# Optimization experiments

Measured on AMD Instinct MI355X. Metric: run time of the kernel, lower is better.

Reference implementation:

```python
import jax, jax.numpy as jnp
import numpy as np

N = 50000      # nodes
E = 800000     # edges (before self-loops)
F_IN = 256     # num_features
H = 4          # heads
C = 64         # hidden_channels
HC = H * C     # 256
L = 2          # n_layers
G = 128        # num graphs
DENSE = 64     # dense_nhid
NCLS = 2       # num_classes
NEG_SLOPE = 0.2
BN_EPS = 1e-5


def setup_inputs() -> dict:
    key = jax.random.key(0)
    ks = jax.random.split(key, 16)
    s = 0.1
    inp = {}
    inp['x'] = jax.random.normal(ks[0], (N, F_IN), jnp.float32)
    inp['edge_index'] = jax.random.randint(ks[1], (2, E), 0, N, dtype=jnp.int32)
    inp['batch'] = jnp.sort(jax.random.randint(ks[2], (N,), 0, G, dtype=jnp.int32))
    # conv1 (GATConv: lin weight [in, H*C], att vectors [H, C], bias [H*C])
    inp['W1'] = jax.random.normal(ks[3], (F_IN, HC), jnp.float32) * s
    inp['as1'] = jax.random.normal(ks[4], (H, C), jnp.float32) * s
    inp['ad1'] = jax.random.normal(ks[5], (H, C), jnp.float32) * s
    inp['b1'] = jnp.zeros((HC,), jnp.float32)
    # stacked params for the L inner conv layers + their BatchNorms
    inp['Wl'] = jax.random.normal(ks[6], (L, HC, HC), jnp.float32) * s
    inp['asl'] = jax.random.normal(ks[7], (L, H, C), jnp.float32) * s
    inp['adl'] = jax.random.normal(ks[8], (L, H, C), jnp.float32) * s
    inp['bl'] = jnp.zeros((L, HC), jnp.float32)
    inp['bng'] = jnp.ones((L, HC), jnp.float32)
    inp['bnb'] = jnp.zeros((L, HC), jnp.float32)
    # bn1 + MLP head
    inp['bn1g'] = jnp.ones((HC,), jnp.float32)
    inp['bn1b'] = jnp.zeros((HC,), jnp.float32)
    inp['lin1W'] = jax.random.normal(ks[9], (HC, DENSE), jnp.float32) * s
    inp['lin1b'] = jnp.zeros((DENSE,), jnp.float32)
    inp['lin2W'] = jax.random.normal(ks[10], (DENSE, DENSE), jnp.float32) * s
    inp['lin2b'] = jnp.zeros((DENSE,), jnp.float32)
    inp['lin3W'] = jax.random.normal(ks[11], (DENSE, NCLS), jnp.float32) * s
    inp['lin3b'] = jnp.zeros((NCLS,), jnp.float32)
    return inp


def _gat(x, src, dst, W, a_src, a_dst, b):
    # GATConv: h_j = W x_j; e_ij = LeakyReLU(a_src.h_j + a_dst.h_i);
    # alpha = softmax over incoming edges of node i; out_i = sum_j alpha*h_j (concat heads) + bias
    h = (x @ W).reshape(-1, H, C)                       # [N, H, C]
    es = jnp.sum(h * a_src, axis=-1)                    # [N, H]
    ed = jnp.sum(h * a_dst, axis=-1)                    # [N, H]
    e = jax.nn.leaky_relu(es[src] + ed[dst], NEG_SLOPE) # [E2, H]
    m = jax.ops.segment_max(e, dst, num_segments=N)
    ex = jnp.exp(e - m[dst])
    ssum = jax.ops.segment_sum(ex, dst, num_segments=N)
    alpha = ex / (ssum[dst] + 1e-16)                    # [E2, H]
    agg = jax.ops.segment_sum(h[src] * alpha[:, :, None], dst, num_segments=N)
    return agg.reshape(-1, HC) + b


def _bn(x, g, b):
    # BatchNorm1d in training mode (biased batch variance)
    mu = jnp.mean(x, axis=0)
    var = jnp.mean((x - mu) ** 2, axis=0)
    return (x - mu) / jnp.sqrt(var + BN_EPS) * g + b


def reference(x, edge_index, batch, W1, as1, ad1, b1, Wl, asl, adl, bl, bng, bnb,
              bn1g, bn1b, lin1W, lin1b, lin2W, lin2b, lin3W, lin3b):
    loops = jnp.arange(N, dtype=edge_index.dtype)
    src = jnp.concatenate([edge_index[0], loops])  # GATConv adds self-loops
    dst = jnp.concatenate([edge_index[1], loops])
    h = jax.nn.relu(_gat(x, src, dst, W1, as1, ad1, b1))
    for i in range(L):
        h = jax.nn.relu(_bn(_gat(h, src, dst, Wl[i], asl[i], adl[i], bl[i]), bng[i], bnb[i]))
    cnt = jax.ops.segment_sum(jnp.ones((N,), h.dtype), batch, num_segments=G)
    pooled = jax.ops.segment_sum(h, batch, num_segments=G) / jnp.maximum(cnt, 1.0)[:, None]
    z = _bn(pooled, bn1g, bn1b)  # dropout is identity in eval
    z = jax.nn.relu(z @ lin1W + lin1b)
    z = jax.nn.relu(z @ lin2W + lin2b)
    z = jax.nn.relu(z @ lin3W + lin3b)
    out = jax.nn.softmax(z, axis=1)
    return (out, pooled)
```

## Files before the change

kernel.cpp:

```cpp
#include <hip/hip_runtime.h>

#define N_NODES 50000
#define E_EDGES 800000
#define E2 (E_EDGES + N_NODES)
#define HC 256
#define NHEAD 4
#define GG 128
#define DENSE 64
#define NCLS 2
#define BN_EPS 1e-5f
#define NEG_SLOPE 0.2f
#define NEG_BIG -1e30f

typedef __attribute__((ext_vector_type(8))) short bf16x8;
typedef __attribute__((ext_vector_type(4))) float f32x4;

__device__ __forceinline__ unsigned short f2bf(float f) {
    unsigned int u = __float_as_uint(f);
    u = (u + 0x7FFFu + ((u >> 16) & 1u)) >> 16;
    return (unsigned short)u;
}
__device__ __forceinline__ float bf2f(unsigned short h) {
    return __uint_as_float(((unsigned int)h) << 16);
}
__device__ __forceinline__ float lrelu(float e) {
    return (e >= 0.f) ? e : NEG_SLOPE * e;
}
__device__ __forceinline__ void accum8(float acc[8], uint4 v, float w) {
    acc[0] = fmaf(w, __uint_as_float(v.x << 16), acc[0]);
    acc[1] = fmaf(w, __uint_as_float(v.x & 0xffff0000u), acc[1]);
    acc[2] = fmaf(w, __uint_as_float(v.y << 16), acc[2]);
    acc[3] = fmaf(w, __uint_as_float(v.y & 0xffff0000u), acc[3]);
    acc[4] = fmaf(w, __uint_as_float(v.z << 16), acc[4]);
    acc[5] = fmaf(w, __uint_as_float(v.z & 0xffff0000u), acc[5]);
    acc[6] = fmaf(w, __uint_as_float(v.w << 16), acc[6]);
    acc[7] = fmaf(w, __uint_as_float(v.w & 0xffff0000u), acc[7]);
}

__global__ __launch_bounds__(256) void convert_bf16_kernel(const float* __restrict__ in,
                                                           unsigned short* __restrict__ out,
                                                           int n8) {
    int i = blockIdx.x * blockDim.x + threadIdx.x;
    if (i >= n8) return;
    const float4* p = reinterpret_cast<const float4*>(in + (size_t)i * 8);
    float4 a = p[0], b = p[1];
    ushort4 lo = make_ushort4(f2bf(a.x), f2bf(a.y), f2bf(a.z), f2bf(a.w));
    ushort4 hi = make_ushort4(f2bf(b.x), f2bf(b.y), f2bf(b.z), f2bf(b.w));
    ushort4* q = reinterpret_cast<ushort4*>(out + (size_t)i * 8);
    q[0] = lo; q[1] = hi;
}

__global__ __launch_bounds__(64) void pack_b_kernel(const float* __restrict__ W,
                                                    unsigned short* __restrict__ Bpk) {
    int l = threadIdx.x;
    int g = blockIdx.x;
    int ks = g >> 4, ct = g & 15;
    int col = ct * 16 + (l & 15);
    int k0 = ks * 32 + (l >> 4) * 8;
    unsigned short v[8];
#pragma unroll
    for (int j = 0; j < 8; ++j) v[j] = f2bf(W[(size_t)(k0 + j) * HC + col]);
    ushort4* q = reinterpret_cast<ushort4*>(Bpk + ((size_t)g * 64 + l) * 8);
    q[0] = make_ushort4(v[0], v[1], v[2], v[3]);
    q[1] = make_ushort4(v[4], v[5], v[6], v[7]);
}

__global__ __launch_bounds__(256) void gemm_mfma_kernel(const unsigned short* __restrict__ A,
                                                        const unsigned short* __restrict__ Bpk,
                                                        unsigned short* __restrict__ C, int M) {
    __shared__ unsigned short As[64 * 256];
    int tid = threadIdx.x;
    int lane = tid & 63, wid = tid >> 6;
    int row0 = blockIdx.x * 64;
#pragma unroll
    for (int i = 0; i < 8; ++i) {
        int idx = tid + i * 256;
        int row = idx >> 5, c16 = idx & 31;
        int grow = row0 + row;
        uint4 v = make_uint4(0u, 0u, 0u, 0u);
        if (grow < M) v = *reinterpret_cast<const uint4*>(A + (size_t)grow * HC + c16 * 8);
        int byteoff = row * 512 + c16 * 16;
        byteoff ^= (row & 7) << 4;
        *reinterpret_cast<uint4*>((char*)As + byteoff) = v;
    }
    __syncthreads();

    f32x4 acc[16];
#pragma unroll
    for (int ct = 0; ct < 16; ++ct) acc[ct] = (f32x4){0.f, 0.f, 0.f, 0.f};

    int mrow = wid * 16 + (lane & 15);
#pragma unroll
    for (int ks = 0; ks < 8; ++ks) {
        int abyte = mrow * 512 + ks * 64 + (lane >> 4) * 16;
        abyte ^= (mrow & 7) << 4;
        bf16x8 a = *reinterpret_cast<const bf16x8*>((char*)As + abyte);
        const unsigned short* bp = Bpk + ((size_t)(ks * 16) * 512 + lane * 8);
#pragma unroll
        for (int ct = 0; ct < 16; ++ct) {
            bf16x8 b = *reinterpret_cast<const bf16x8*>(bp + (size_t)ct * 512);
            acc[ct] = __builtin_amdgcn_mfma_f32_16x16x32_bf16(a, b, acc[ct], 0, 0, 0);
        }
    }
    int crow0 = row0 + wid * 16 + (lane >> 4) * 4;
    int ccol = lane & 15;
#pragma unroll
    for (int ct = 0; ct < 16; ++ct) {
#pragma unroll
        for (int r = 0; r < 4; ++r) {
            int grow = crow0 + r;
            if (grow < M) C[(size_t)grow * HC + ct * 16 + ccol] = f2bf(acc[ct][r]);
        }
    }
}

__global__ __launch_bounds__(256) void esed_kernel(const unsigned short* __restrict__ h,
                                                   const float* __restrict__ avs,
                                                   const float* __restrict__ avd,
                                                   float* __restrict__ es, float* __restrict__ ed) {
    int tid = threadIdx.x;
    int lane = tid & 63, wid = tid >> 6;
    int node = blockIdx.x * 4 + wid;
    if (node >= N_NODES) return;
    int ch0 = lane * 4;
    ushort4 hv = *reinterpret_cast<const ushort4*>(h + (size_t)node * HC + ch0);
    float4 sa = *reinterpret_cast<const float4*>(avs + ch0);
    float4 da = *reinterpret_cast<const float4*>(avd + ch0);
    float h0 = bf2f(hv.x), h1 = bf2f(hv.y), h2 = bf2f(hv.z), h3 = bf2f(hv.w);
    float vs = h0 * sa.x + h1 * sa.y + h2 * sa.z + h3 * sa.w;
    float vd = h0 * da.x + h1 * da.y + h2 * da.z + h3 * da.w;
#pragma unroll
    for (int m = 1; m < 16; m <<= 1) {
        vs += __shfl_xor(vs, m, 64);
        vd += __shfl_xor(vd, m, 64);
    }
    if ((lane & 15) == 0) {
        es[node * NHEAD + (lane >> 4)] = vs;
        ed[node * NHEAD + (lane >> 4)] = vd;
    }
}

__global__ void init_deg_kernel(int* __restrict__ deg) {
    int i = blockIdx.x * blockDim.x + threadIdx.x;
    if (i < N_NODES) deg[i] = 1;
}
__global__ void count_edges_kernel(const int* __restrict__ dst, int* __restrict__ deg) {
    int i = blockIdx.x * blockDim.x + threadIdx.x;
    if (i < E_EDGES) atomicAdd(&deg[dst[i]], 1);
}
__global__ __launch_bounds__(1024) void scan1_kernel(const int* __restrict__ deg,
                                                     int* __restrict__ rs, int* __restrict__ bsum) {
    __shared__ int wsum[16];
    int t = threadIdx.x, lane = t & 63, wid = t >> 6;
    int i = blockIdx.x * 1024 + t;
    int v = (i < N_NODES) ? deg[i] : 0;
    int x = v;
#pragma unroll
    for (int off = 1; off < 64; off <<= 1) {
        int y = __shfl_up(x, off, 64);
        if (lane >= off) x += y;
    }
    if (lane == 63) wsum[wid] = x;
    __syncthreads();
    if (wid == 0) {
        int s = (lane < 16) ? wsum[lane] : 0;
#pragma unroll
        for (int off = 1; off < 16; off <<= 1) {
            int y = __shfl_up(s, off, 64);
            if (lane >= off) s += y;
        }
        if (lane < 16) wsum[lane] = s;
    }
    __syncthreads();
    int woff = wid ? wsum[wid - 1] : 0;
    if (i <= N_NODES) rs[i] = woff + x - v;
    if (t == 1023) bsum[blockIdx.x] = wsum[15];
}
__global__ void scan2_kernel(int* __restrict__ bsum, int nb) {
    int l = threadIdx.x;
    int v = (l < nb) ? bsum[l] : 0;
    int x = v;
#pragma unroll
    for (int off = 1; off < 64; off <<= 1) {
        int y = __shfl_up(x, off, 64);
        if (l >= off) x += y;
    }
    if (l < nb) bsum[l] = x - v;
}
__global__ void scan3_kernel(int* __restrict__ rs, const int* __restrict__ bsum,
                             int* __restrict__ cursor) {
    int i = blockIdx.x * blockDim.x + threadIdx.x;
    if (i <= N_NODES) {
        int v = rs[i] + bsum[i >> 10];
        rs[i] = v;
        if (i < N_NODES) cursor[i] = v;
    }
}
__global__ void scatter_self_kernel(int* __restrict__ cursor, int* __restrict__ csr) {
    int i = blockIdx.x * blockDim.x + threadIdx.x;
    if (i < N_NODES) {
        int pos = atomicAdd(&cursor[i], 1);
        csr[pos] = i;
    }
}
__global__ void scatter_edges_kernel(const int* __restrict__ src, const int* __restrict__ dst,
                                     int* __restrict__ cursor, int* __restrict__ csr) {
    int i = blockIdx.x * blockDim.x + threadIdx.x;
    if (i < E_EDGES) {
        int pos = atomicAdd(&cursor[dst[i]], 1);
        csr[pos] = src[i];
    }
}

__global__ __launch_bounds__(256) void smprep_kernel(const float* __restrict__ es,
                                                     const float* __restrict__ ed,
                                                     const int* __restrict__ rs,
                                                     const int* __restrict__ csr,
                                                     float* __restrict__ alpha) {
    int tid = threadIdx.x;
    int lane = tid & 63, wid = tid >> 6;
    int node = blockIdx.x * 4 + wid;
    if (node >= N_NODES) return;
    int head = lane >> 4, slot = lane & 15;
    float edn = ed[node * NHEAD + head];
    int beg = rs[node], end = rs[node + 1];
    float m = NEG_BIG, s = 0.f;
    for (int i = beg + slot; i < end; i += 16) {
        float e = lrelu(es[csr[i] * NHEAD + head] + edn);
        alpha[(size_t)i * NHEAD + head] = e;
        float mn = fmaxf(m, e);
        s = s * __expf(m - mn) + __expf(e - mn);
        m = mn;
    }
#pragma unroll
    for (int off = 1; off < 16; off <<= 1) {
        float mo = __shfl_xor(m, off, 64);
        float so = __shfl_xor(s, off, 64);
        float mn = fmaxf(m, mo);
        s = s * __expf(m - mn) + so * __expf(mo - mn);
        m = mn;
    }
    float inv = 1.f / (s + 1e-16f);
    for (int i = beg + slot; i < end; i += 16) {
        float e = alpha[(size_t)i * NHEAD + head];
        alpha[(size_t)i * NHEAD + head] = __expf(e - m) * inv;
    }
}

__global__ __launch_bounds__(256) void gat_agg_kernel(const unsigned short* __restrict__ hlin,
                                                      const float* __restrict__ alpha,
                                                      const int* __restrict__ rs,
                                                      const int* __restrict__ csr,
                                                      const float* __restrict__ bias,
                                                      unsigned short* __restrict__ out, int do_relu) {
    int tid = threadIdx.x;
    int lane = tid & 63, wid = tid >> 6;
    int node = blockIdx.x * 8 + wid * 2 + (lane >> 5);
    int hl = lane & 31;
    int ch0 = hl * 8;
    int head = hl >> 3;
    bool valid = node < N_NODES;
    int beg = valid ? rs[node] : 0;
    int end = valid ? rs[node + 1] : 0;
    float acc[8] = {};
    int idx = beg;
    for (; idx + 4 <= end; idx += 4) {
        int s0 = csr[idx], s1 = csr[idx + 1], s2 = csr[idx + 2], s3 = csr[idx + 3];
        float p0 = alpha[(size_t)idx * NHEAD + head];
        float p1 = alpha[(size_t)(idx + 1) * NHEAD + head];
        float p2 = alpha[(size_t)(idx + 2) * NHEAD + head];
        float p3 = alpha[(size_t)(idx + 3) * NHEAD + head];
        uint4 v0 = *reinterpret_cast<const uint4*>(hlin + (size_t)s0 * HC + ch0);
        uint4 v1 = *reinterpret_cast<const uint4*>(hlin + (size_t)s1 * HC + ch0);
        uint4 v2 = *reinterpret_cast<const uint4*>(hlin + (size_t)s2 * HC + ch0);
        uint4 v3 = *reinterpret_cast<const uint4*>(hlin + (size_t)s3 * HC + ch0);
        accum8(acc, v0, p0);
        accum8(acc, v1, p1);
        accum8(acc, v2, p2);
        accum8(acc, v3, p3);
    }
    for (; idx < end; ++idx) {
        int s0 = csr[idx];
        float p0 = alpha[(size_t)idx * NHEAD + head];
        uint4 v0 = *reinterpret_cast<const uint4*>(hlin + (size_t)s0 * HC + ch0);
        accum8(acc, v0, p0);
    }
    if (!valid) return;
    const float4 bva = *reinterpret_cast<const float4*>(bias + ch0);
    const float4 bvb = *reinterpret_cast<const float4*>(bias + ch0 + 4);
    float o[8];
    o[0] = acc[0] + bva.x; o[1] = acc[1] + bva.y; o[2] = acc[2] + bva.z; o[3] = acc[3] + bva.w;
    o[4] = acc[4] + bvb.x; o[5] = acc[5] + bvb.y; o[6] = acc[6] + bvb.z; o[7] = acc[7] + bvb.w;
    if (do_relu) {
#pragma unroll
        for (int j = 0; j < 8; ++j) o[j] = fmaxf(o[j], 0.f);
    }
    uint4 w;
    w.x = (unsigned int)f2bf(o[0]) | ((unsigned int)f2bf(o[1]) << 16);
    w.y = (unsigned int)f2bf(o[2]) | ((unsigned int)f2bf(o[3]) << 16);
    w.z = (unsigned int)f2bf(o[4]) | ((unsigned int)f2bf(o[5]) << 16);
    w.w = (unsigned int)f2bf(o[6]) | ((unsigned int)f2bf(o[7]) << 16);
    *reinterpret_cast<uint4*>(out + (size_t)node * HC + ch0) = w;
}

#define BN_RPB 49
__global__ __launch_bounds__(256) void bn_stats_kernel(const unsigned short* __restrict__ x,
                                                       float* __restrict__ sums) {
    __shared__ float lds[8][512];
    int tid = threadIdx.x;
    int c = tid & 31;
    int rt = tid >> 5;
    int r0 = blockIdx.x * BN_RPB;
    int r1 = min(N_NODES, r0 + BN_RPB);
    int ch = c * 8;
    float s[8] = {}, s2[8] = {};
    for (int r = r0 + rt; r < r1; r += 8) {
        const ushort4* p = reinterpret_cast<const ushort4*>(x + (size_t)r * HC + ch);
        ushort4 va = p[0], vb = p[1];
        unsigned short in[8] = {va.x, va.y, va.z, va.w, vb.x, vb.y, vb.z, vb.w};
#pragma unroll
        for (int j = 0; j < 8; ++j) {
            float v = bf2f(in[j]);
            s[j] += v; s2[j] += v * v;
        }
    }
#pragma unroll
    for (int j = 0; j < 8; ++j) {
        lds[rt][ch + j] = s[j];
        lds[rt][256 + ch + j] = s2[j];
    }
    __syncthreads();
#pragma unroll
    for (int e = tid; e < 512; e += 256) {
        float v = 0.f;
#pragma unroll
        for (int r = 0; r < 8; ++r) v += lds[r][e];
        atomicAdd(&sums[e], v);
    }
}
__global__ void bn_finalize_kernel(const float* __restrict__ sums, const float* __restrict__ g,
                                   const float* __restrict__ b, float* __restrict__ prm) {
    int t = threadIdx.x;
    float mean = sums[t] / (float)N_NODES;
    float var = sums[HC + t] / (float)N_NODES - mean * mean;
    var = fmaxf(var, 0.f);
    float scale = g[t] * rsqrtf(var + BN_EPS);
    prm[t] = scale;
    prm[HC + t] = b[t] - mean * scale;
}
__global__ __launch_bounds__(256) void bn_apply_relu_kernel(const unsigned short* __restrict__ x,
                                                            const float* __restrict__ prm,
                                                            unsigned short* __restrict__ out) {
    int i = blockIdx.x * blockDim.x + threadIdx.x;
    const int total8 = N_NODES * HC / 8;
    if (i >= total8) return;
    int c0 = (i * 8) & (HC - 1);
    const ushort4* p = reinterpret_cast<const ushort4*>(x + (size_t)i * 8);
    ushort4 va = p[0], vb = p[1];
    unsigned short o[8];
    unsigned short in[8] = {va.x, va.y, va.z, va.w, vb.x, vb.y, vb.z, vb.w};
#pragma unroll
    for (int j = 0; j < 8; ++j) {
        float v = bf2f(in[j]) * prm[c0 + j] + prm[HC + c0 + j];
        o[j] = f2bf(fmaxf(v, 0.f));
    }
    ushort4* q = reinterpret_cast<ushort4*>(out + (size_t)i * 8);
    q[0] = make_ushort4(o[0], o[1], o[2], o[3]);
    q[1] = make_ushort4(o[4], o[5], o[6], o[7]);
}

__global__ __launch_bounds__(GG) void graph_ub_kernel(const int* __restrict__ batch,
                                                      int* __restrict__ ub) {
    int g = threadIdx.x;
    int lo = 0, hi = N_NODES;
    while (lo < hi) {
        int mid = (lo + hi) >> 1;
        if (batch[mid] <= g) lo = mid + 1; else hi = mid;
    }
    ub[g] = lo;
}
#define POOL_RPB 32
__global__ __launch_bounds__(256) void pool_kernel(const unsigned short* __restrict__ h,
                                                   const int* __restrict__ batch,
                                                   float* __restrict__ psum) {
    int tid = threadIdx.x;
    int ct = tid & 63;
    int rt = tid >> 6;
    int r0 = blockIdx.x * POOL_RPB;
    int r1 = min(N_NODES, r0 + POOL_RPB);
    int ch = ct * 4;
    float a0 = 0.f, a1 = 0.f, a2 = 0.f, a3 = 0.f;
    int gcur = -1;
    for (int r = r0 + rt; r < r1; r += 4) {
        int g = batch[r];
        if (g != gcur) {
            if (gcur >= 0) {
                atomicAdd(&psum[gcur * HC + ch + 0], a0);
                atomicAdd(&psum[gcur * HC + ch + 1], a1);
                atomicAdd(&psum[gcur * HC + ch + 2], a2);
                atomicAdd(&psum[gcur * HC + ch + 3], a3);
            }
            a0 = a1 = a2 = a3 = 0.f; gcur = g;
        }
        ushort4 hv = *reinterpret_cast<const ushort4*>(h + (size_t)r * HC + ch);
        a0 += bf2f(hv.x); a1 += bf2f(hv.y); a2 += bf2f(hv.z); a3 += bf2f(hv.w);
    }
    if (gcur >= 0) {
        atomicAdd(&psum[gcur * HC + ch + 0], a0);
        atomicAdd(&psum[gcur * HC + ch + 1], a1);
        atomicAdd(&psum[gcur * HC + ch + 2], a2);
        atomicAdd(&psum[gcur * HC + ch + 3], a3);
    }
}
__global__ void pool_fin_kernel(const float* __restrict__ psum, const int* __restrict__ ub,
                                float* __restrict__ pooled) {
    int g = blockIdx.x, t = threadIdx.x;
    int c = ub[g] - (g > 0 ? ub[g - 1] : 0);
    float cf = fmaxf((float)c, 1.f);
    pooled[g * HC + t] = psum[g * HC + t] / cf;
}

__global__ __launch_bounds__(256) void bn_head_kernel(const float* __restrict__ pooled,
                                                      const float* __restrict__ g,
                                                      const float* __restrict__ b,
                                                      float* __restrict__ z) {
    int t = threadIdx.x;
    float s = 0.f, s2 = 0.f;
    for (int r = 0; r < GG; ++r) {
        float v = pooled[r * HC + t];
        s += v; s2 += v * v;
    }
    float mean = s / (float)GG;
    float var = fmaxf(s2 / (float)GG - mean * mean, 0.f);
    float scale = g[t] * rsqrtf(var + BN_EPS);
    float shift = b[t] - mean * scale;
    for (int r = 0; r < GG; ++r)
        z[r * HC + t] = pooled[r * HC + t] * scale + shift;
}
__global__ __launch_bounds__(64) void lin_relu_kernel(const float* __restrict__ X,
                                                      const float* __restrict__ W,
                                                      const float* __restrict__ b,
                                                      float* __restrict__ Y, int K) {
    __shared__ float xr[256];
    int r = blockIdx.x, t = threadIdx.x;
    for (int k = t; k < K; k += 64) xr[k] = X[r * K + k];
    __syncthreads();
    float a = b[t];
    for (int k = 0; k < K; ++k) a += xr[k] * W[k * DENSE + t];
    Y[r * DENSE + t] = fmaxf(a, 0.f);
}
__global__ __launch_bounds__(128) void lin3_softmax_kernel(const float* __restrict__ X,
                                                           const float* __restrict__ W,
                                                           const float* __restrict__ b,
                                                           float* __restrict__ out) {
    int r = threadIdx.x;
    const float* xr = X + r * DENSE;
    float o0 = b[0], o1 = b[1];
    for (int k = 0; k < DENSE; ++k) {
        o0 += xr[k] * W[k * NCLS + 0];
        o1 += xr[k] * W[k * NCLS + 1];
    }
    o0 = fmaxf(o0, 0.f); o1 = fmaxf(o1, 0.f);
    float mx = fmaxf(o0, o1);
    float e0 = __expf(o0 - mx), e1 = __expf(o1 - mx);
    float inv = 1.f / (e0 + e1);
    out[r * NCLS + 0] = e0 * inv;
    out[r * NCLS + 1] = e1 * inv;
}

extern "C" void kernel_launch(void* const* d_in, const int* in_sizes, int n_in,
                              void* d_out, int out_size, void* d_ws, size_t ws_size,
                              hipStream_t stream) {
    const float* x     = (const float*)d_in[0];
    const int*   ei    = (const int*)d_in[1];
    const int*   srcp  = ei;
    const int*   dstp  = ei + E_EDGES;
    const int*   batch = (const int*)d_in[2];
    const float* W1    = (const float*)d_in[3];
    const float* as1   = (const float*)d_in[4];
    const float* ad1   = (const float*)d_in[5];
    const float* b1    = (const float*)d_in[6];
    const float* Wl    = (const float*)d_in[7];
    const float* asl   = (const float*)d_in[8];
    const float* adl   = (const float*)d_in[9];
    const float* bl    = (const float*)d_in[10];
    const float* bng   = (const float*)d_in[11];
    const float* bnb   = (const float*)d_in[12];
    const float* bn1g  = (const float*)d_in[13];
    const float* bn1b  = (const float*)d_in[14];
    const float* l1W   = (const float*)d_in[15];
    const float* l1b   = (const float*)d_in[16];
    const float* l2W   = (const float*)d_in[17];
    const float* l2b   = (const float*)d_in[18];
    const float* l3W   = (const float*)d_in[19];
    const float* l3b   = (const float*)d_in[20];

    float* outp   = (float*)d_out;
    float* pooled = outp + GG * NCLS;

    char* w = (char*)d_ws;
    auto alloc = [&](size_t bytes) -> void* {
        void* p = (void*)w;
        w += (bytes + 255) & ~(size_t)255;
        return p;
    };
    unsigned short* xb  = (unsigned short*)alloc(sizeof(short) * (size_t)N_NODES * HC);
    unsigned short* h0  = (unsigned short*)alloc(sizeof(short) * (size_t)N_NODES * HC);
    unsigned short* h1  = (unsigned short*)alloc(sizeof(short) * (size_t)N_NODES * HC);
    unsigned short* h2  = (unsigned short*)alloc(sizeof(short) * (size_t)N_NODES * HC);
    unsigned short* Bpk = (unsigned short*)alloc(sizeof(short) * 3 * 128 * 64 * 8);
    float* es     = (float*)alloc(sizeof(float) * (size_t)N_NODES * NHEAD);
    float* ed     = (float*)alloc(sizeof(float) * (size_t)N_NODES * NHEAD);
    float* alpha  = (float*)alloc(sizeof(float) * (size_t)E2 * NHEAD);
    int*   rs     = (int*)alloc(sizeof(int) * (N_NODES + 1));
    int*   deg    = (int*)alloc(sizeof(int) * N_NODES);
    int*   csr    = (int*)alloc(sizeof(int) * E2);
    int*   bsum   = (int*)alloc(sizeof(int) * 64);
    float* bnsums = (float*)alloc(sizeof(float) * 2 * HC);
    float* bnprm  = (float*)alloc(sizeof(float) * 2 * HC);
    float* psum   = (float*)alloc(sizeof(float) * GG * HC);
    int*   ub     = (int*)alloc(sizeof(int) * GG);
    float* z0     = (float*)alloc(sizeof(float) * GG * HC);
    float* z1     = (float*)alloc(sizeof(float) * GG * DENSE);
    float* z2     = (float*)alloc(sizeof(float) * GG * DENSE);

    const int nblk_nodes = (N_NODES + 255) / 256;
    const int nblk_edges = (E_EDGES + 255) / 256;
    const int nblk_wave4 = (N_NODES + 3) / 4;
    const int nblk_wave8 = (N_NODES + 7) / 8;
    const int nscan = (N_NODES + 1023) / 1024;
    const int nblk_bn   = (N_NODES + BN_RPB - 1) / BN_RPB;
    const int nblk_pool = (N_NODES + POOL_RPB - 1) / POOL_RPB;

    pack_b_kernel<<<128, 64, 0, stream>>>(W1, Bpk);
    pack_b_kernel<<<128, 64, 0, stream>>>(Wl, Bpk + 128 * 64 * 8);
    pack_b_kernel<<<128, 64, 0, stream>>>(Wl + (size_t)HC * HC, Bpk + 2 * 128 * 64 * 8);
    convert_bf16_kernel<<<(N_NODES * HC / 8 + 255) / 256, 256, 0, stream>>>(x, xb, N_NODES * HC / 8);

    init_deg_kernel<<<nblk_nodes, 256, 0, stream>>>(deg);
    count_edges_kernel<<<nblk_edges, 256, 0, stream>>>(dstp, deg);
    scan1_kernel<<<nscan, 1024, 0, stream>>>(deg, rs, bsum);
    scan2_kernel<<<1, 64, 0, stream>>>(bsum, nscan);
    scan3_kernel<<<(N_NODES + 256) / 256, 256, 0, stream>>>(rs, bsum, deg);
    scatter_self_kernel<<<nblk_nodes, 256, 0, stream>>>(deg, csr);
    scatter_edges_kernel<<<nblk_edges, 256, 0, stream>>>(srcp, dstp, deg, csr);

    const int ggrid = (N_NODES + 63) / 64;

    gemm_mfma_kernel<<<ggrid, 256, 0, stream>>>(xb, Bpk, h1, N_NODES);
    esed_kernel<<<nblk_wave4, 256, 0, stream>>>(h1, as1, ad1, es, ed);
    smprep_kernel<<<nblk_wave4, 256, 0, stream>>>(es, ed, rs, csr, alpha);
    gat_agg_kernel<<<nblk_wave8, 256, 0, stream>>>(h1, alpha, rs, csr, b1, h0, 1);

    for (int i = 0; i < 2; ++i) {
        gemm_mfma_kernel<<<ggrid, 256, 0, stream>>>(h0, Bpk + (size_t)(i + 1) * 128 * 64 * 8, h1, N_NODES);
        esed_kernel<<<nblk_wave4, 256, 0, stream>>>(h1, asl + i * HC, adl + i * HC, es, ed);
        smprep_kernel<<<nblk_wave4, 256, 0, stream>>>(es, ed, rs, csr, alpha);
        gat_agg_kernel<<<nblk_wave8, 256, 0, stream>>>(h1, alpha, rs, csr, bl + i * HC, h2, 0);
        hipMemsetAsync(bnsums, 0, sizeof(float) * 2 * HC, stream);
        bn_stats_kernel<<<nblk_bn, 256, 0, stream>>>(h2, bnsums);
        bn_finalize_kernel<<<1, 256, 0, stream>>>(bnsums, bng + i * HC, bnb + i * HC, bnprm);
        bn_apply_relu_kernel<<<(N_NODES * HC / 8 + 255) / 256, 256, 0, stream>>>(h2, bnprm, h0);
    }

    hipMemsetAsync(psum, 0, sizeof(float) * GG * HC, stream);
    graph_ub_kernel<<<1, GG, 0, stream>>>(batch, ub);
    pool_kernel<<<nblk_pool, 256, 0, stream>>>(h0, batch, psum);
    pool_fin_kernel<<<GG, HC, 0, stream>>>(psum, ub, pooled);

    bn_head_kernel<<<1, HC, 0, stream>>>(pooled, bn1g, bn1b, z0);
    lin_relu_kernel<<<GG, 64, 0, stream>>>(z0, l1W, l1b, z1, HC);
    lin_relu_kernel<<<GG, 64, 0, stream>>>(z1, l2W, l2b, z2, DENSE);
    lin3_softmax_kernel<<<1, GG, 0, stream>>>(z2, l3W, l3b, outp);
}
```

Baseline: 621.1 us.

## Fuse BN-apply+ReLU into next GEMM load and pooling; merge self-loop scatter

Removes the standalone BatchNorm apply+ReLU pass by applying the scale/shift and ReLU while loading A tiles in the next layer's GEMM, and inside the pooling kernel for the last layer. This avoids one full read and write of the 50000x256 bf16 activation per layer. Self-loop CSR insertion moves into the scan kernel, which drops one launch and its atomics. The aggregation loop is also unrolled by 8 so more gathers are in flight, at the cost of extra registers.

```diff
diff --git a/kernel.cpp b/kernel.cpp
--- a/kernel.cpp
+++ b/kernel.cpp
@@ -67,6 +67,7 @@
 
 __global__ __launch_bounds__(256) void gemm_mfma_kernel(const unsigned short* __restrict__ A,
                                                         const unsigned short* __restrict__ Bpk,
+                                                        const float* __restrict__ prm,
                                                         unsigned short* __restrict__ C, int M) {
     __shared__ unsigned short As[64 * 256];
     int tid = threadIdx.x;
@@ -79,6 +80,25 @@
         int grow = row0 + row;
         uint4 v = make_uint4(0u, 0u, 0u, 0u);
         if (grow < M) v = *reinterpret_cast<const uint4*>(A + (size_t)grow * HC + c16 * 8);
+        if (prm) {
+            int ch = c16 * 8;
+            const float4 s0 = *reinterpret_cast<const float4*>(prm + ch);
+            const float4 s1 = *reinterpret_cast<const float4*>(prm + ch + 4);
+            const float4 t0 = *reinterpret_cast<const float4*>(prm + HC + ch);
+            const float4 t1 = *reinterpret_cast<const float4*>(prm + HC + ch + 4);
+            float f0 = fmaxf(fmaf(__uint_as_float(v.x << 16),          s0.x, t0.x), 0.f);
+            float f1 = fmaxf(fmaf(__uint_as_float(v.x & 0xffff0000u),  s0.y, t0.y), 0.f);
+            float f2 = fmaxf(fmaf(__uint_as_float(v.y << 16),          s0.z, t0.z), 0.f);
+            float f3 = fmaxf(fmaf(__uint_as_float(v.y & 0xffff0000u),  s0.w, t0.w), 0.f);
+            float f4 = fmaxf(fmaf(__uint_as_float(v.z << 16),          s1.x, t1.x), 0.f);
+            float f5 = fmaxf(fmaf(__uint_as_float(v.z & 0xffff0000u),  s1.y, t1.y), 0.f);
+            float f6 = fmaxf(fmaf(__uint_as_float(v.w << 16),          s1.z, t1.z), 0.f);
+            float f7 = fmaxf(fmaf(__uint_as_float(v.w & 0xffff0000u),  s1.w, t1.w), 0.f);
+            v.x = (unsigned int)f2bf(f0) | ((unsigned int)f2bf(f1) << 16);
+            v.y = (unsigned int)f2bf(f2) | ((unsigned int)f2bf(f3) << 16);
+            v.z = (unsigned int)f2bf(f4) | ((unsigned int)f2bf(f5) << 16);
+            v.w = (unsigned int)f2bf(f6) | ((unsigned int)f2bf(f7) << 16);
+        }
         int byteoff = row * 512 + c16 * 16;
         byteoff ^= (row & 7) << 4;
         *reinterpret_cast<uint4*>((char*)As + byteoff) = v;
@@ -188,19 +208,15 @@
     if (l < nb) bsum[l] = x - v;
 }
 __global__ void scan3_kernel(int* __restrict__ rs, const int* __restrict__ bsum,
-                             int* __restrict__ cursor) {
+                             int* __restrict__ cursor, int* __restrict__ csr) {
     int i = blockIdx.x * blockDim.x + threadIdx.x;
     if (i <= N_NODES) {
         int v = rs[i] + bsum[i >> 10];
         rs[i] = v;
-        if (i < N_NODES) cursor[i] = v;
-    }
-}
-__global__ void scatter_self_kernel(int* __restrict__ cursor, int* __restrict__ csr) {
-    int i = blockIdx.x * blockDim.x + threadIdx.x;
-    if (i < N_NODES) {
-        int pos = atomicAdd(&cursor[i], 1);
-        csr[pos] = i;
+        if (i < N_NODES) {
+            csr[v] = i;
+            cursor[i] = v + 1;
+        }
     }
 }
 __global__ void scatter_edges_kernel(const int* __restrict__ src, const int* __restrict__ dst,
@@ -264,7 +280,21 @@
     int end = valid ? rs[node + 1] : 0;
     float acc[8] = {};
     int idx = beg;
-    for (; idx + 4 <= end; idx += 4) {
+    for (; idx + 8 <= end; idx += 8) {
+        int si[8]; float pi[8];
+#pragma unroll
+        for (int j = 0; j < 8; ++j) {
+            si[j] = csr[idx + j];
+            pi[j] = alpha[(size_t)(idx + j) * NHEAD + head];
+        }
+        uint4 v[8];
+#pragma unroll
+        for (int j = 0; j < 8; ++j)
+            v[j] = *reinterpret_cast<const uint4*>(hlin + (size_t)si[j] * HC + ch0);
+#pragma unroll
+        for (int j = 0; j < 8; ++j) accum8(acc, v[j], pi[j]);
+    }
+    if (idx + 4 <= end) {
         int s0 = csr[idx], s1 = csr[idx + 1], s2 = csr[idx + 2], s3 = csr[idx + 3];
         float p0 = alpha[(size_t)idx * NHEAD + head];
         float p1 = alpha[(size_t)(idx + 1) * NHEAD + head];
@@ -278,6 +308,7 @@
         accum8(acc, v1, p1);
         accum8(acc, v2, p2);
         accum8(acc, v3, p3);
+        idx += 4;
     }
     for (; idx < end; ++idx) {
         int s0 = csr[idx];
@@ -348,26 +379,6 @@
     prm[t] = scale;
     prm[HC + t] = b[t] - mean * scale;
 }
-__global__ __launch_bounds__(256) void bn_apply_relu_kernel(const unsigned short* __restrict__ x,
-                                                            const float* __restrict__ prm,
-                                                            unsigned short* __restrict__ out) {
-    int i = blockIdx.x * blockDim.x + threadIdx.x;
-    const int total8 = N_NODES * HC / 8;
-    if (i >= total8) return;
-    int c0 = (i * 8) & (HC - 1);
-    const ushort4* p = reinterpret_cast<const ushort4*>(x + (size_t)i * 8);
-    ushort4 va = p[0], vb = p[1];
-    unsigned short o[8];
-    unsigned short in[8] = {va.x, va.y, va.z, va.w, vb.x, vb.y, vb.z, vb.w};
-#pragma unroll
-    for (int j = 0; j < 8; ++j) {
-        float v = bf2f(in[j]) * prm[c0 + j] + prm[HC + c0 + j];
-        o[j] = f2bf(fmaxf(v, 0.f));
-    }
-    ushort4* q = reinterpret_cast<ushort4*>(out + (size_t)i * 8);
-    q[0] = make_ushort4(o[0], o[1], o[2], o[3]);
-    q[1] = make_ushort4(o[4], o[5], o[6], o[7]);
-}
 
 __global__ __launch_bounds__(GG) void graph_ub_kernel(const int* __restrict__ batch,
                                                       int* __restrict__ ub) {
@@ -381,6 +392,7 @@
 }
 #define POOL_RPB 32
 __global__ __launch_bounds__(256) void pool_kernel(const unsigned short* __restrict__ h,
+                                                   const float* __restrict__ prm,
                                                    const int* __restrict__ batch,
                                                    float* __restrict__ psum) {
     int tid = threadIdx.x;
@@ -389,6 +401,8 @@
     int r0 = blockIdx.x * POOL_RPB;
     int r1 = min(N_NODES, r0 + POOL_RPB);
     int ch = ct * 4;
+    const float4 sc = *reinterpret_cast<const float4*>(prm + ch);
+    const float4 sh = *reinterpret_cast<const float4*>(prm + HC + ch);
     float a0 = 0.f, a1 = 0.f, a2 = 0.f, a3 = 0.f;
     int gcur = -1;
     for (int r = r0 + rt; r < r1; r += 4) {
@@ -403,7 +417,10 @@
             a0 = a1 = a2 = a3 = 0.f; gcur = g;
         }
         ushort4 hv = *reinterpret_cast<const ushort4*>(h + (size_t)r * HC + ch);
-        a0 += bf2f(hv.x); a1 += bf2f(hv.y); a2 += bf2f(hv.z); a3 += bf2f(hv.w);
+        a0 += fmaxf(fmaf(bf2f(hv.x), sc.x, sh.x), 0.f);
+        a1 += fmaxf(fmaf(bf2f(hv.y), sc.y, sh.y), 0.f);
+        a2 += fmaxf(fmaf(bf2f(hv.z), sc.z, sh.z), 0.f);
+        a3 += fmaxf(fmaf(bf2f(hv.w), sc.w, sh.w), 0.f);
     }
     if (gcur >= 0) {
         atomicAdd(&psum[gcur * HC + ch + 0], a0);
@@ -541,31 +558,35 @@
     count_edges_kernel<<<nblk_edges, 256, 0, stream>>>(dstp, deg);
     scan1_kernel<<<nscan, 1024, 0, stream>>>(deg, rs, bsum);
     scan2_kernel<<<1, 64, 0, stream>>>(bsum, nscan);
-    scan3_kernel<<<(N_NODES + 256) / 256, 256, 0, stream>>>(rs, bsum, deg);
-    scatter_self_kernel<<<nblk_nodes, 256, 0, stream>>>(deg, csr);
+    scan3_kernel<<<(N_NODES + 256) / 256, 256, 0, stream>>>(rs, bsum, deg, csr);
     scatter_edges_kernel<<<nblk_edges, 256, 0, stream>>>(srcp, dstp, deg, csr);
 
     const int ggrid = (N_NODES + 63) / 64;
 
-    gemm_mfma_kernel<<<ggrid, 256, 0, stream>>>(xb, Bpk, h1, N_NODES);
+    gemm_mfma_kernel<<<ggrid, 256, 0, stream>>>(xb, Bpk, nullptr, h1, N_NODES);
     esed_kernel<<<nblk_wave4, 256, 0, stream>>>(h1, as1, ad1, es, ed);
     smprep_kernel<<<nblk_wave4, 256, 0, stream>>>(es, ed, rs, csr, alpha);
     gat_agg_kernel<<<nblk_wave8, 256, 0, stream>>>(h1, alpha, rs, csr, b1, h0, 1);
 
-    for (int i = 0; i < 2; ++i) {
-        gemm_mfma_kernel<<<ggrid, 256, 0, stream>>>(h0, Bpk + (size_t)(i + 1) * 128 * 64 * 8, h1, N_NODES);
-        esed_kernel<<<nblk_wave4, 256, 0, stream>>>(h1, asl + i * HC, adl + i * HC, es, ed);
-        smprep_kernel<<<nblk_wave4, 256, 0, stream>>>(es, ed, rs, csr, alpha);
-        gat_agg_kernel<<<nblk_wave8, 256, 0, stream>>>(h1, alpha, rs, csr, bl + i * HC, h2, 0);
-        hipMemsetAsync(bnsums, 0, sizeof(float) * 2 * HC, stream);
-        bn_stats_kernel<<<nblk_bn, 256, 0, stream>>>(h2, bnsums);
-        bn_finalize_kernel<<<1, 256, 0, stream>>>(bnsums, bng + i * HC, bnb + i * HC, bnprm);
-        bn_apply_relu_kernel<<<(N_NODES * HC / 8 + 255) / 256, 256, 0, stream>>>(h2, bnprm, h0);
-    }
+    gemm_mfma_kernel<<<ggrid, 256, 0, stream>>>(h0, Bpk + 128 * 64 * 8, nullptr, h1, N_NODES);
+    esed_kernel<<<nblk_wave4, 256, 0, stream>>>(h1, asl, adl, es, ed);
+    smprep_kernel<<<nblk_wave4, 256, 0, stream>>>(es, ed, rs, csr, alpha);
+    gat_agg_kernel<<<nblk_wave8, 256, 0, stream>>>(h1, alpha, rs, csr, bl, h2, 0);
+    hipMemsetAsync(bnsums, 0, sizeof(float) * 2 * HC, stream);
+    bn_stats_kernel<<<nblk_bn, 256, 0, stream>>>(h2, bnsums);
+    bn_finalize_kernel<<<1, 256, 0, stream>>>(bnsums, bng, bnb, bnprm);
+
+    gemm_mfma_kernel<<<ggrid, 256, 0, stream>>>(h2, Bpk + 2 * 128 * 64 * 8, bnprm, h1, N_NODES);
+    esed_kernel<<<nblk_wave4, 256, 0, stream>>>(h1, asl + HC, adl + HC, es, ed);
+    smprep_kernel<<<nblk_wave4, 256, 0, stream>>>(es, ed, rs, csr, alpha);
+    gat_agg_kernel<<<nblk_wave8, 256, 0, stream>>>(h1, alpha, rs, csr, bl + HC, h2, 0);
+    hipMemsetAsync(bnsums, 0, sizeof(float) * 2 * HC, stream);
+    bn_stats_kernel<<<nblk_bn, 256, 0, stream>>>(h2, bnsums);
+    bn_finalize_kernel<<<1, 256, 0, stream>>>(bnsums, bng + HC, bnb + HC, bnprm);
 
     hipMemsetAsync(psum, 0, sizeof(float) * GG * HC, stream);
     graph_ub_kernel<<<1, GG, 0, stream>>>(batch, ub);
-    pool_kernel<<<nblk_pool, 256, 0, stream>>>(h0, batch, psum);
+    pool_kernel<<<nblk_pool, 256, 0, stream>>>(h2, bnprm, batch, psum);
     pool_fin_kernel<<<GG, HC, 0, stream>>>(psum, ub, pooled);
 
     bn_head_kernel<<<1, HC, 0, stream>>>(pooled, bn1g, bn1b, z0);
```

After: 607.0 us. -2.3%, faster.
